# Kernel optimization log

Hardware: AMD Instinct MI355X
Metric: run time of the kernel (lower is better)

## Reference

```python
import jax, jax.numpy as jnp
import numpy as np

N_NODES = 100000
N_EDGES = 3200000
N_FEAT = 128
EMB = 64


def setup_inputs() -> dict:
    key = jax.random.key(0)
    ks = jax.random.split(key, 10)
    x = jax.random.normal(ks[0], (N_NODES, N_FEAT), dtype=jnp.float32)
    edge_index = jax.random.randint(ks[1], (2, N_EDGES), 0, N_NODES, dtype=jnp.int64)
    batch_index = jnp.zeros((N_NODES,), dtype=jnp.int64)
    def glorot(k, fan_in, fan_out):
        s = jnp.sqrt(2.0 / (fan_in + fan_out)).astype(jnp.float32)
        return jax.random.normal(k, (fan_in, fan_out), dtype=jnp.float32) * s
    return {
        "x": x,
        "edge_index": edge_index,
        "batch_index": batch_index,
        "W0": glorot(ks[2], N_FEAT, EMB), "b0": jnp.zeros((EMB,), jnp.float32),
        "W1": glorot(ks[3], EMB, EMB),    "b1": jnp.zeros((EMB,), jnp.float32),
        "W2": glorot(ks[4], EMB, EMB),    "b2": jnp.zeros((EMB,), jnp.float32),
        "W3": glorot(ks[5], EMB, EMB),    "b3": jnp.zeros((EMB,), jnp.float32),
        "Wout": glorot(ks[6], EMB, 1),    "bout": jnp.zeros((1,), jnp.float32),
    }


def _gcn_norm(edge_index, n_nodes):
    # Add self-loops, compute symmetric normalization D^{-1/2} A_hat D^{-1/2}.
    loops = jnp.arange(n_nodes, dtype=edge_index.dtype)
    src = jnp.concatenate([edge_index[0], loops])  # message sources
    dst = jnp.concatenate([edge_index[1], loops])  # aggregation targets
    ones = jnp.ones(src.shape[0], dtype=jnp.float32)
    deg = jax.ops.segment_sum(ones, dst, num_segments=n_nodes)
    dinv = jnp.where(deg > 0, jax.lax.rsqrt(deg), 0.0)
    norm = dinv[src] * dinv[dst]  # [E + N]
    return src, dst, norm


def _gcn_conv(h, src, dst, norm, W, b, n_nodes):
    h = h @ W                              # [N, out]
    msg = h[src] * norm[:, None]           # gather + scale
    agg = jax.ops.segment_sum(msg, dst, num_segments=n_nodes)  # scatter-add
    return agg + b


def reference(x, edge_index, batch_index, W0, b0, W1, b1, W2, b2, W3, b3, Wout, bout):
    n = x.shape[0]
    src, dst, norm = _gcn_norm(edge_index, n)
    y = _gcn_conv(x, src, dst, norm, W0, b0, n)
    y = _gcn_conv(y, src, dst, norm, W1, b1, n)
    y = _gcn_conv(y, src, dst, norm, W2, b2, n)
    y = _gcn_conv(y, src, dst, norm, W3, b3, n)
    out = y @ Wout + bout
    return (out, y)
```

## Files before the change

### kernel.cpp

```cpp
#include <hip/hip_runtime.h>
#include <hip/hip_fp16.h>


#define FEAT 128
#define EMB 64
#define BINSHIFT 8
#define BINSIZE 256
#define NBIN 391
#define CHUNK 8192


__global__ __launch_bounds__(256) void bin_count_k(
    const int* __restrict__ dst, int* __restrict__ bincnt, int E) {
    __shared__ int hist[NBIN];
    int t = threadIdx.x;
    int base = blockIdx.x * CHUNK;
    int end = min(base + CHUNK, E);
    for (int i = t; i < NBIN; i += 256) hist[i] = 0;
    __syncthreads();
    for (int e = base + t; e < end; e += 256)
        atomicAdd(&hist[dst[e] >> BINSHIFT], 1);
    __syncthreads();
    for (int b = t; b < NBIN; b += 256) {
        int c = hist[b];
        if (c > 0) atomicAdd(&bincnt[b], c);
    }
}

__global__ void binscan_k(const int* __restrict__ bincnt, int* __restrict__ binptr,
                          int* __restrict__ bincur, int nbin, int E) {
    __shared__ int s[512];
    int t = threadIdx.x;
    int v = (t < nbin) ? bincnt[t] : 0;
    s[t] = v;
    __syncthreads();
    for (int off = 1; off < 512; off <<= 1) {
        int tv = (t >= off) ? s[t - off] : 0;
        __syncthreads();
        s[t] += tv;
        __syncthreads();
    }
    if (t < nbin) {
        int excl = s[t] - v;
        binptr[t] = excl;
        bincur[t] = excl;
    }
    if (t == 0) binptr[nbin] = E;
}

__global__ __launch_bounds__(256) void bin_edges_k(
    const int* __restrict__ src, const int* __restrict__ dst,
    int* __restrict__ bincur, int* __restrict__ ebuf, int E) {
    __shared__ int hist[NBIN];
    __shared__ int lcur[NBIN];
    int t = threadIdx.x;
    int base = blockIdx.x * CHUNK;
    int end = min(base + CHUNK, E);
    for (int i = t; i < NBIN; i += 256) hist[i] = 0;
    __syncthreads();
    for (int e = base + t; e < end; e += 256)
        atomicAdd(&hist[dst[e] >> BINSHIFT], 1);
    __syncthreads();
    for (int b = t; b < NBIN; b += 256) {
        int c = hist[b];
        lcur[b] = (c > 0) ? atomicAdd(&bincur[b], c) : 0;
    }
    __syncthreads();
    for (int e = base + t; e < end; e += 256) {
        int d = dst[e];
        int bin = d >> BINSHIFT;
        int r = atomicAdd(&lcur[bin], 1);
        ebuf[r] = src[e] | ((d & (BINSIZE - 1)) << 24);
    }
}

__global__ __launch_bounds__(256) void build_csr_k(
    const int* __restrict__ ebuf, const int* __restrict__ binptr,
    int* __restrict__ rowptr, float* __restrict__ dinv,
    int* __restrict__ col, int N, int E, int nbin) {
    __shared__ int lcnt[BINSIZE];
    __shared__ int lscan[BINSIZE];
    __shared__ int lcur[BINSIZE];
    int b = blockIdx.x;
    int t = threadIdx.x;
    int n0 = b << BINSHIFT;
    int e0 = binptr[b];
    int e1 = binptr[b + 1];

    lcnt[t] = 0;
    __syncthreads();
    for (int i = e0 + t; i < e1; i += 256)
        atomicAdd(&lcnt[((unsigned)ebuf[i]) >> 24], 1);
    __syncthreads();

    int v = lcnt[t];
    lscan[t] = v;
    __syncthreads();
    for (int off = 1; off < 256; off <<= 1) {
        int tv = (t >= off) ? lscan[t - off] : 0;
        __syncthreads();
        lscan[t] += tv;
        __syncthreads();
    }
    int excl = e0 + lscan[t] - v;
    lcur[t] = excl;
    if (n0 + t < N) {
        rowptr[n0 + t] = excl;
        dinv[n0 + t] = 1.0f / sqrtf((float)(v + 1));
    }
    if (b == nbin - 1 && t == 0) rowptr[N] = E;
    __syncthreads();

    for (int i = e0 + t; i < e1; i += 256) {
        int w = ebuf[i];
        int dl = ((unsigned)w) >> 24;
        int p = atomicAdd(&lcur[dl], 1);
        col[p] = (w & 0xFFFFFF) << 7;
    }
}

template <int K>
__global__ __launch_bounds__(256, 4) void gemm_scale_k(
    const float* __restrict__ H, const float* __restrict__ W,
    const float* __restrict__ dinv, __half* __restrict__ G, int N) {
    __shared__ float Ws[K * EMB];
    int t = threadIdx.x;
    for (int i = t * 4; i < K * EMB; i += 1024) {
        *(float4*)(Ws + i) = *(const float4*)(W + i);
    }
    __syncthreads();

    int tc = t & 15;
    int tr = t >> 4;
    int j0 = tc * 4;
    int r0 = blockIdx.x * 64 + tr * 4;
    if (r0 >= N) return;

    const float* hp[4];
#pragma unroll
    for (int i = 0; i < 4; i++) {
        int r = (r0 + i < N) ? (r0 + i) : (N - 1);
        hp[i] = H + (size_t)r * K;
    }

    float acc[4][4] = {{0.f}};
    float4 a[4], an[4];
#pragma unroll
    for (int i = 0; i < 4; i++) a[i] = *(const float4*)(hp[i]);

#pragma unroll 1
    for (int k = 0; k < K; k += 4) {
        if (k + 4 < K) {
#pragma unroll
            for (int i = 0; i < 4; i++) an[i] = *(const float4*)(hp[i] + k + 4);
        }
#pragma unroll
        for (int kk = 0; kk < 4; kk++) {
            float4 wv = *(const float4*)(Ws + (k + kk) * EMB + j0);
#pragma unroll
            for (int i = 0; i < 4; i++) {
                float av = (kk == 0) ? a[i].x : (kk == 1) ? a[i].y : (kk == 2) ? a[i].z : a[i].w;
                acc[i][0] = fmaf(av, wv.x, acc[i][0]);
                acc[i][1] = fmaf(av, wv.y, acc[i][1]);
                acc[i][2] = fmaf(av, wv.z, acc[i][2]);
                acc[i][3] = fmaf(av, wv.w, acc[i][3]);
            }
        }
#pragma unroll
        for (int i = 0; i < 4; i++) a[i] = an[i];
    }

#pragma unroll
    for (int i = 0; i < 4; i++) {
        if (r0 + i < N) {
            float s = dinv[r0 + i];
            union { __half2 h2[2]; float2 f2; } o;
            o.h2[0] = __floats2half2_rn(acc[i][0] * s, acc[i][1] * s);
            o.h2[1] = __floats2half2_rn(acc[i][2] * s, acc[i][3] * s);
            *(float2*)(G + (size_t)(r0 + i) * EMB + j0) = o.f2;
        }
    }
}


__device__ __forceinline__ void h8_acc(float (&a)[8], float4 raw) {
    union { float4 f4; __half2 h2[4]; } u;
    u.f4 = raw;
    float2 p0 = __half22float2(u.h2[0]);
    float2 p1 = __half22float2(u.h2[1]);
    float2 p2 = __half22float2(u.h2[2]);
    float2 p3 = __half22float2(u.h2[3]);
    a[0] += p0.x; a[1] += p0.y; a[2] += p1.x; a[3] += p1.y;
    a[4] += p2.x; a[5] += p2.y; a[6] += p3.x; a[7] += p3.y;
}

__device__ __forceinline__ void agg_node8(const __half* __restrict__ G,
                                          const int* __restrict__ coff,
                                          int s, int e, int selfoff,
                                          int grp, int f8, float (&r)[8]) {
    const char* Gb = (const char*)G + f8 * 16;
    float a0[8] = {0.f, 0.f, 0.f, 0.f, 0.f, 0.f, 0.f, 0.f};
    float a1[8] = {0.f, 0.f, 0.f, 0.f, 0.f, 0.f, 0.f, 0.f};
    float a2[8] = {0.f, 0.f, 0.f, 0.f, 0.f, 0.f, 0.f, 0.f};
    float a3[8] = {0.f, 0.f, 0.f, 0.f, 0.f, 0.f, 0.f, 0.f};
    if (grp == 0) h8_acc(a0, *(const float4*)(Gb + selfoff));

    int i = s;
    if (i + 32 <= e) {
        int c0 = coff[i + grp];
        int c1 = coff[i + 8 + grp];
        int c2 = coff[i + 16 + grp];
        int c3 = coff[i + 24 + grp];
        while (true) {
            float4 g0 = *(const float4*)(Gb + (size_t)(unsigned)c0);
            float4 g1 = *(const float4*)(Gb + (size_t)(unsigned)c1);
            float4 g2 = *(const float4*)(Gb + (size_t)(unsigned)c2);
            float4 g3 = *(const float4*)(Gb + (size_t)(unsigned)c3);
            i += 32;
            bool more = (i + 32 <= e);
            if (more) {
                c0 = coff[i + grp];
                c1 = coff[i + 8 + grp];
                c2 = coff[i + 16 + grp];
                c3 = coff[i + 24 + grp];
            }
            h8_acc(a0, g0);
            h8_acc(a1, g1);
            h8_acc(a2, g2);
            h8_acc(a3, g3);
            if (!more) break;
        }
    }
    for (; i + 8 <= e; i += 8) {
        float4 g = *(const float4*)(Gb + (size_t)(unsigned)coff[i + grp]);
        h8_acc(a1, g);
    }
    if (grp < e - i) {
        float4 g = *(const float4*)(Gb + (size_t)(unsigned)coff[i + grp]);
        h8_acc(a2, g);
    }

#pragma unroll
    for (int k = 0; k < 8; k++) {
        float v = (a0[k] + a1[k]) + (a2[k] + a3[k]);
        v += __shfl_xor(v, 8, 64);
        v += __shfl_xor(v, 16, 64);
        v += __shfl_xor(v, 32, 64);
        r[k] = v;
    }
}

__global__ __launch_bounds__(256) void agg_k(
    const __half* __restrict__ G, const float* __restrict__ dinv,
    const int* __restrict__ rowptr, const int* __restrict__ coff,
    const float* __restrict__ bias, float* __restrict__ Hout, int N) {
    int gw = (blockIdx.x * 256 + threadIdx.x) >> 6;
    int lane = threadIdx.x & 63;
    if (gw >= N) return;
    gw = __builtin_amdgcn_readfirstlane(gw);
    int grp = lane >> 3;
    int f8 = lane & 7;
    int s = rowptr[gw], e = rowptr[gw + 1];
    float r[8];
    agg_node8(G, coff, s, e, gw << 7, grp, f8, r);
    if (grp == 0) {
        float d = dinv[gw];
        float4 b0v = *(const float4*)(bias + f8 * 8);
        float4 b1v = *(const float4*)(bias + f8 * 8 + 4);
        float4 lo = make_float4(r[0] * d + b0v.x, r[1] * d + b0v.y,
                                r[2] * d + b0v.z, r[3] * d + b0v.w);
        float4 hi = make_float4(r[4] * d + b1v.x, r[5] * d + b1v.y,
                                r[6] * d + b1v.z, r[7] * d + b1v.w);
        float* o = Hout + (size_t)gw * EMB + f8 * 8;
        *(float4*)o = lo;
        *(float4*)(o + 4) = hi;
    }
}

__global__ __launch_bounds__(256) void agg_final_k(
    const __half* __restrict__ G, const float* __restrict__ dinv,
    const int* __restrict__ rowptr, const int* __restrict__ coff,
    const float* __restrict__ bias, const float* __restrict__ Wout,
    const float* __restrict__ bout, float* __restrict__ Y,
    float* __restrict__ Out, int N) {
    int gw = (blockIdx.x * 256 + threadIdx.x) >> 6;
    int lane = threadIdx.x & 63;
    if (gw >= N) return;
    gw = __builtin_amdgcn_readfirstlane(gw);
    int grp = lane >> 3;
    int f8 = lane & 7;
    int s = rowptr[gw], e = rowptr[gw + 1];
    float r[8];
    agg_node8(G, coff, s, e, gw << 7, grp, f8, r);
    float d = dinv[gw];
    float4 b0v = *(const float4*)(bias + f8 * 8);
    float4 b1v = *(const float4*)(bias + f8 * 8 + 4);
    float v0 = r[0] * d + b0v.x, v1 = r[1] * d + b0v.y;
    float v2 = r[2] * d + b0v.z, v3 = r[3] * d + b0v.w;
    float v4 = r[4] * d + b1v.x, v5 = r[5] * d + b1v.y;
    float v6 = r[6] * d + b1v.z, v7 = r[7] * d + b1v.w;
    if (grp == 0) {
        float* o = Y + (size_t)gw * EMB + f8 * 8;
        *(float4*)o = make_float4(v0, v1, v2, v3);
        *(float4*)(o + 4) = make_float4(v4, v5, v6, v7);
    }
    float4 w0v = *(const float4*)(Wout + f8 * 8);
    float4 w1v = *(const float4*)(Wout + f8 * 8 + 4);
    float p = v0 * w0v.x + v1 * w0v.y + v2 * w0v.z + v3 * w0v.w +
              v4 * w1v.x + v5 * w1v.y + v6 * w1v.z + v7 * w1v.w;
    p += __shfl_xor(p, 1, 8);
    p += __shfl_xor(p, 2, 8);
    p += __shfl_xor(p, 4, 8);
    if (lane == 0) Out[gw] = p + bout[0];
}


extern "C" void kernel_launch(void* const* d_in, const int* in_sizes, int n_in,
                              void* d_out, int out_size, void* d_ws, size_t ws_size,
                              hipStream_t stream) {
    const float* x    = (const float*)d_in[0];
    const int*   ei   = (const int*)d_in[1];
    const float* W0   = (const float*)d_in[3];
    const float* b0   = (const float*)d_in[4];
    const float* W1   = (const float*)d_in[5];
    const float* b1   = (const float*)d_in[6];
    const float* W2   = (const float*)d_in[7];
    const float* b2   = (const float*)d_in[8];
    const float* W3   = (const float*)d_in[9];
    const float* b3   = (const float*)d_in[10];
    const float* Wout = (const float*)d_in[11];
    const float* bout = (const float*)d_in[12];

    const int N = in_sizes[0] / FEAT;
    const int E = in_sizes[1] / 2;
    const int* srcp = ei;
    const int* dstp = ei + E;
    const int nbin = (N + BINSIZE - 1) / BINSIZE;

    const int NP = ((N + 64) + 63) / 64 * 64;
    float* dinv  = (float*)d_ws;
    int* rowptr  = (int*)(dinv + NP);
    int* bincnt  = rowptr + NP;
    int* binptr  = bincnt + 1024;
    int* bincur  = binptr + 1024;
    int* col     = bincur + 1024;
    float* bufA  = (float*)(col + ((E + 63) / 64) * 64);
    int* ebuf    = (int*)bufA;
    __half* Gbuf = (__half*)bufA;

    float* Out = (float*)d_out;
    float* Y   = Out + N;

    const int gemm_blocks = (N + 63) / 64;
    const int agg_blocks  = (N + 3) / 4;
    const int nchunk = (E + CHUNK - 1) / CHUNK;

    hipMemsetAsync(bincnt, 0, 1024 * sizeof(int), stream);
    bin_count_k<<<nchunk, 256, 0, stream>>>(dstp, bincnt, E);
    binscan_k<<<1, 512, 0, stream>>>(bincnt, binptr, bincur, nbin, E);
    bin_edges_k<<<nchunk, 256, 0, stream>>>(srcp, dstp, bincur, ebuf, E);
    build_csr_k<<<nbin, 256, 0, stream>>>(ebuf, binptr, rowptr, dinv, col, N, E, nbin);

    gemm_scale_k<FEAT><<<gemm_blocks, 256, 0, stream>>>(x, W0, dinv, Gbuf, N);
    agg_k<<<agg_blocks, 256, 0, stream>>>(Gbuf, dinv, rowptr, col, b0, Y, N);
    gemm_scale_k<EMB><<<gemm_blocks, 256, 0, stream>>>(Y, W1, dinv, Gbuf, N);
    agg_k<<<agg_blocks, 256, 0, stream>>>(Gbuf, dinv, rowptr, col, b1, Y, N);
    gemm_scale_k<EMB><<<gemm_blocks, 256, 0, stream>>>(Y, W2, dinv, Gbuf, N);
    agg_k<<<agg_blocks, 256, 0, stream>>>(Gbuf, dinv, rowptr, col, b2, Y, N);
    gemm_scale_k<EMB><<<gemm_blocks, 256, 0, stream>>>(Y, W3, dinv, Gbuf, N);
    agg_final_k<<<agg_blocks, 256, 0, stream>>>(Gbuf, dinv, rowptr, col, b3, Wout, bout,
                                                Y, Out, N);
}
```

Measured before the change: 579.3 us.

## Fuse the GEMM and aggregation layers into one persistent cooperative kernel

The four GEMM+scale kernels and four aggregation kernels are replaced by a single persistent cooperative kernel. It loops over row tiles and node groups with grid-stride loops and separates the phases with grid.sync. This removes seven kernel launches and their inter-kernel gaps. In exchange the grid is capped at four 256-thread blocks per CU because of the 32 KB shared weight buffer, which lowers occupancy for the gather-heavy aggregation, and each of the seven grid barriers adds its own cost.

```diff
diff --git a/kernel.cpp b/kernel.cpp
--- a/kernel.cpp
+++ b/kernel.cpp
@@ -1,5 +1,8 @@
 #include <hip/hip_runtime.h>
 #include <hip/hip_fp16.h>
+#include <hip/hip_cooperative_groups.h>
+
+namespace cg = cooperative_groups;
 
 
 #define FEAT 128
@@ -119,65 +122,84 @@
     }
 }
 
+
+struct FusedArgs {
+    const float* x;
+    const float* W0; const float* b0;
+    const float* W1; const float* b1;
+    const float* W2; const float* b2;
+    const float* W3; const float* b3;
+    const float* Wout; const float* bout;
+    const float* dinv;
+    const int* rowptr;
+    const int* coff;
+    __half* G;
+    float* Y;
+    float* Out;
+    int N;
+};
+
 template <int K>
-__global__ __launch_bounds__(256, 4) void gemm_scale_k(
+__device__ __forceinline__ void gemm_phase(
     const float* __restrict__ H, const float* __restrict__ W,
-    const float* __restrict__ dinv, __half* __restrict__ G, int N) {
-    __shared__ float Ws[K * EMB];
+    const float* __restrict__ dinv, __half* __restrict__ G,
+    int N, float* Ws) {
     int t = threadIdx.x;
-    for (int i = t * 4; i < K * EMB; i += 1024) {
+    for (int i = t * 4; i < K * EMB; i += 1024)
         *(float4*)(Ws + i) = *(const float4*)(W + i);
-    }
     __syncthreads();
 
     int tc = t & 15;
     int tr = t >> 4;
     int j0 = tc * 4;
-    int r0 = blockIdx.x * 64 + tr * 4;
-    if (r0 >= N) return;
-
-    const float* hp[4];
-#pragma unroll
-    for (int i = 0; i < 4; i++) {
-        int r = (r0 + i < N) ? (r0 + i) : (N - 1);
-        hp[i] = H + (size_t)r * K;
-    }
-
-    float acc[4][4] = {{0.f}};
-    float4 a[4], an[4];
-#pragma unroll
-    for (int i = 0; i < 4; i++) a[i] = *(const float4*)(hp[i]);
+    int ntile = (N + 63) >> 6;
+
+    for (int tile = blockIdx.x; tile < ntile; tile += gridDim.x) {
+        int r0 = tile * 64 + tr * 4;
+        const float* hp[4];
+#pragma unroll
+        for (int i = 0; i < 4; i++) {
+            int r = (r0 + i < N) ? (r0 + i) : (N - 1);
+            hp[i] = H + (size_t)r * K;
+        }
+
+        float acc[4][4] = {{0.f}};
+        float4 a[4], an[4];
+#pragma unroll
+        for (int i = 0; i < 4; i++) a[i] = *(const float4*)(hp[i]);
 
 #pragma unroll 1
-    for (int k = 0; k < K; k += 4) {
-        if (k + 4 < K) {
-#pragma unroll
-            for (int i = 0; i < 4; i++) an[i] = *(const float4*)(hp[i] + k + 4);
-        }
-#pragma unroll
-        for (int kk = 0; kk < 4; kk++) {
-            float4 wv = *(const float4*)(Ws + (k + kk) * EMB + j0);
-#pragma unroll
-            for (int i = 0; i < 4; i++) {
-                float av = (kk == 0) ? a[i].x : (kk == 1) ? a[i].y : (kk == 2) ? a[i].z : a[i].w;
-                acc[i][0] = fmaf(av, wv.x, acc[i][0]);
-                acc[i][1] = fmaf(av, wv.y, acc[i][1]);
-                acc[i][2] = fmaf(av, wv.z, acc[i][2]);
-                acc[i][3] = fmaf(av, wv.w, acc[i][3]);
+        for (int k = 0; k < K; k += 4) {
+            if (k + 4 < K) {
+#pragma unroll
+                for (int i = 0; i < 4; i++) an[i] = *(const float4*)(hp[i] + k + 4);
             }
-        }
-#pragma unroll
-        for (int i = 0; i < 4; i++) a[i] = an[i];
-    }
-
-#pragma unroll
-    for (int i = 0; i < 4; i++) {
-        if (r0 + i < N) {
-            float s = dinv[r0 + i];
-            union { __half2 h2[2]; float2 f2; } o;
-            o.h2[0] = __floats2half2_rn(acc[i][0] * s, acc[i][1] * s);
-            o.h2[1] = __floats2half2_rn(acc[i][2] * s, acc[i][3] * s);
-            *(float2*)(G + (size_t)(r0 + i) * EMB + j0) = o.f2;
+#pragma unroll
+            for (int kk = 0; kk < 4; kk++) {
+                float4 wv = *(const float4*)(Ws + (k + kk) * EMB + j0);
+#pragma unroll
+                for (int i = 0; i < 4; i++) {
+                    float av = (kk == 0) ? a[i].x : (kk == 1) ? a[i].y
+                             : (kk == 2) ? a[i].z : a[i].w;
+                    acc[i][0] = fmaf(av, wv.x, acc[i][0]);
+                    acc[i][1] = fmaf(av, wv.y, acc[i][1]);
+                    acc[i][2] = fmaf(av, wv.z, acc[i][2]);
+                    acc[i][3] = fmaf(av, wv.w, acc[i][3]);
+                }
+            }
+#pragma unroll
+            for (int i = 0; i < 4; i++) a[i] = an[i];
+        }
+
+#pragma unroll
+        for (int i = 0; i < 4; i++) {
+            if (r0 + i < N) {
+                float s = dinv[r0 + i];
+                union { __half2 h2[2]; float2 f2; } o;
+                o.h2[0] = __floats2half2_rn(acc[i][0] * s, acc[i][1] * s);
+                o.h2[1] = __floats2half2_rn(acc[i][2] * s, acc[i][3] * s);
+                *(float2*)(G + (size_t)(r0 + i) * EMB + j0) = o.f2;
+            }
         }
     }
 }
@@ -250,68 +272,98 @@
     }
 }
 
-__global__ __launch_bounds__(256) void agg_k(
+__device__ __forceinline__ void agg_phase(
     const __half* __restrict__ G, const float* __restrict__ dinv,
     const int* __restrict__ rowptr, const int* __restrict__ coff,
     const float* __restrict__ bias, float* __restrict__ Hout, int N) {
-    int gw = (blockIdx.x * 256 + threadIdx.x) >> 6;
+    int wid = threadIdx.x >> 6;
     int lane = threadIdx.x & 63;
-    if (gw >= N) return;
-    gw = __builtin_amdgcn_readfirstlane(gw);
     int grp = lane >> 3;
     int f8 = lane & 7;
-    int s = rowptr[gw], e = rowptr[gw + 1];
-    float r[8];
-    agg_node8(G, coff, s, e, gw << 7, grp, f8, r);
-    if (grp == 0) {
-        float d = dinv[gw];
-        float4 b0v = *(const float4*)(bias + f8 * 8);
-        float4 b1v = *(const float4*)(bias + f8 * 8 + 4);
-        float4 lo = make_float4(r[0] * d + b0v.x, r[1] * d + b0v.y,
-                                r[2] * d + b0v.z, r[3] * d + b0v.w);
-        float4 hi = make_float4(r[4] * d + b1v.x, r[5] * d + b1v.y,
-                                r[6] * d + b1v.z, r[7] * d + b1v.w);
-        float* o = Hout + (size_t)gw * EMB + f8 * 8;
-        *(float4*)o = lo;
-        *(float4*)(o + 4) = hi;
-    }
-}
-
-__global__ __launch_bounds__(256) void agg_final_k(
+    int ngrp = (N + 3) >> 2;
+    for (int gq = blockIdx.x; gq < ngrp; gq += gridDim.x) {
+        int gw = gq * 4 + wid;
+        if (gw >= N) continue;
+        gw = __builtin_amdgcn_readfirstlane(gw);
+        int s = rowptr[gw], e = rowptr[gw + 1];
+        float r[8];
+        agg_node8(G, coff, s, e, gw << 7, grp, f8, r);
+        if (grp == 0) {
+            float d = dinv[gw];
+            float4 b0v = *(const float4*)(bias + f8 * 8);
+            float4 b1v = *(const float4*)(bias + f8 * 8 + 4);
+            float4 lo = make_float4(r[0] * d + b0v.x, r[1] * d + b0v.y,
+                                    r[2] * d + b0v.z, r[3] * d + b0v.w);
+            float4 hi = make_float4(r[4] * d + b1v.x, r[5] * d + b1v.y,
+                                    r[6] * d + b1v.z, r[7] * d + b1v.w);
+            float* o = Hout + (size_t)gw * EMB + f8 * 8;
+            *(float4*)o = lo;
+            *(float4*)(o + 4) = hi;
+        }
+    }
+}
+
+__device__ __forceinline__ void agg_final_phase(
     const __half* __restrict__ G, const float* __restrict__ dinv,
     const int* __restrict__ rowptr, const int* __restrict__ coff,
     const float* __restrict__ bias, const float* __restrict__ Wout,
     const float* __restrict__ bout, float* __restrict__ Y,
     float* __restrict__ Out, int N) {
-    int gw = (blockIdx.x * 256 + threadIdx.x) >> 6;
+    int wid = threadIdx.x >> 6;
     int lane = threadIdx.x & 63;
-    if (gw >= N) return;
-    gw = __builtin_amdgcn_readfirstlane(gw);
     int grp = lane >> 3;
     int f8 = lane & 7;
-    int s = rowptr[gw], e = rowptr[gw + 1];
-    float r[8];
-    agg_node8(G, coff, s, e, gw << 7, grp, f8, r);
-    float d = dinv[gw];
-    float4 b0v = *(const float4*)(bias + f8 * 8);
-    float4 b1v = *(const float4*)(bias + f8 * 8 + 4);
-    float v0 = r[0] * d + b0v.x, v1 = r[1] * d + b0v.y;
-    float v2 = r[2] * d + b0v.z, v3 = r[3] * d + b0v.w;
-    float v4 = r[4] * d + b1v.x, v5 = r[5] * d + b1v.y;
-    float v6 = r[6] * d + b1v.z, v7 = r[7] * d + b1v.w;
-    if (grp == 0) {
-        float* o = Y + (size_t)gw * EMB + f8 * 8;
-        *(float4*)o = make_float4(v0, v1, v2, v3);
-        *(float4*)(o + 4) = make_float4(v4, v5, v6, v7);
-    }
-    float4 w0v = *(const float4*)(Wout + f8 * 8);
-    float4 w1v = *(const float4*)(Wout + f8 * 8 + 4);
-    float p = v0 * w0v.x + v1 * w0v.y + v2 * w0v.z + v3 * w0v.w +
-              v4 * w1v.x + v5 * w1v.y + v6 * w1v.z + v7 * w1v.w;
-    p += __shfl_xor(p, 1, 8);
-    p += __shfl_xor(p, 2, 8);
-    p += __shfl_xor(p, 4, 8);
-    if (lane == 0) Out[gw] = p + bout[0];
+    int ngrp = (N + 3) >> 2;
+    for (int gq = blockIdx.x; gq < ngrp; gq += gridDim.x) {
+        int gw = gq * 4 + wid;
+        if (gw >= N) continue;
+        gw = __builtin_amdgcn_readfirstlane(gw);
+        int s = rowptr[gw], e = rowptr[gw + 1];
+        float r[8];
+        agg_node8(G, coff, s, e, gw << 7, grp, f8, r);
+        float d = dinv[gw];
+        float4 b0v = *(const float4*)(bias + f8 * 8);
+        float4 b1v = *(const float4*)(bias + f8 * 8 + 4);
+        float v0 = r[0] * d + b0v.x, v1 = r[1] * d + b0v.y;
+        float v2 = r[2] * d + b0v.z, v3 = r[3] * d + b0v.w;
+        float v4 = r[4] * d + b1v.x, v5 = r[5] * d + b1v.y;
+        float v6 = r[6] * d + b1v.z, v7 = r[7] * d + b1v.w;
+        if (grp == 0) {
+            float* o = Y + (size_t)gw * EMB + f8 * 8;
+            *(float4*)o = make_float4(v0, v1, v2, v3);
+            *(float4*)(o + 4) = make_float4(v4, v5, v6, v7);
+        }
+        float4 w0v = *(const float4*)(Wout + f8 * 8);
+        float4 w1v = *(const float4*)(Wout + f8 * 8 + 4);
+        float p = v0 * w0v.x + v1 * w0v.y + v2 * w0v.z + v3 * w0v.w +
+                  v4 * w1v.x + v5 * w1v.y + v6 * w1v.z + v7 * w1v.w;
+        p += __shfl_xor(p, 1, 8);
+        p += __shfl_xor(p, 2, 8);
+        p += __shfl_xor(p, 4, 8);
+        if (lane == 0) Out[gw] = p + bout[0];
+    }
+}
+
+__global__ __launch_bounds__(256, 4) void fused_k(FusedArgs A) {
+    cg::grid_group grid = cg::this_grid();
+    __shared__ float Ws[FEAT * EMB];
+
+    gemm_phase<FEAT>(A.x, A.W0, A.dinv, A.G, A.N, Ws);
+    grid.sync();
+    agg_phase(A.G, A.dinv, A.rowptr, A.coff, A.b0, A.Y, A.N);
+    grid.sync();
+    gemm_phase<EMB>(A.Y, A.W1, A.dinv, A.G, A.N, Ws);
+    grid.sync();
+    agg_phase(A.G, A.dinv, A.rowptr, A.coff, A.b1, A.Y, A.N);
+    grid.sync();
+    gemm_phase<EMB>(A.Y, A.W2, A.dinv, A.G, A.N, Ws);
+    grid.sync();
+    agg_phase(A.G, A.dinv, A.rowptr, A.coff, A.b2, A.Y, A.N);
+    grid.sync();
+    gemm_phase<EMB>(A.Y, A.W3, A.dinv, A.G, A.N, Ws);
+    grid.sync();
+    agg_final_phase(A.G, A.dinv, A.rowptr, A.coff, A.b3, A.Wout, A.bout,
+                    A.Y, A.Out, A.N);
 }
 
 
@@ -351,8 +403,6 @@
     float* Out = (float*)d_out;
     float* Y   = Out + N;
 
-    const int gemm_blocks = (N + 63) / 64;
-    const int agg_blocks  = (N + 3) / 4;
     const int nchunk = (E + CHUNK - 1) / CHUNK;
 
     hipMemsetAsync(bincnt, 0, 1024 * sizeof(int), stream);
@@ -361,13 +411,30 @@
     bin_edges_k<<<nchunk, 256, 0, stream>>>(srcp, dstp, bincur, ebuf, E);
     build_csr_k<<<nbin, 256, 0, stream>>>(ebuf, binptr, rowptr, dinv, col, N, E, nbin);
 
-    gemm_scale_k<FEAT><<<gemm_blocks, 256, 0, stream>>>(x, W0, dinv, Gbuf, N);
-    agg_k<<<agg_blocks, 256, 0, stream>>>(Gbuf, dinv, rowptr, col, b0, Y, N);
-    gemm_scale_k<EMB><<<gemm_blocks, 256, 0, stream>>>(Y, W1, dinv, Gbuf, N);
-    agg_k<<<agg_blocks, 256, 0, stream>>>(Gbuf, dinv, rowptr, col, b1, Y, N);
-    gemm_scale_k<EMB><<<gemm_blocks, 256, 0, stream>>>(Y, W2, dinv, Gbuf, N);
-    agg_k<<<agg_blocks, 256, 0, stream>>>(Gbuf, dinv, rowptr, col, b2, Y, N);
-    gemm_scale_k<EMB><<<gemm_blocks, 256, 0, stream>>>(Y, W3, dinv, Gbuf, N);
-    agg_final_k<<<agg_blocks, 256, 0, stream>>>(Gbuf, dinv, rowptr, col, b3, Wout, bout,
-                                                Y, Out, N);
-}
+    static int nblk = 0;
+    if (nblk == 0) {
+        int bpc = 0;
+        hipError_t err = hipOccupancyMaxActiveBlocksPerMultiprocessor(
+            &bpc, (const void*)fused_k, 256, 0);
+        if (err != hipSuccess || bpc < 1) bpc = 4;
+        if (bpc > 4) bpc = 4;
+        nblk = bpc * 256;
+    }
+    FusedArgs fa;
+    fa.x = x;
+    fa.W0 = W0; fa.b0 = b0;
+    fa.W1 = W1; fa.b1 = b1;
+    fa.W2 = W2; fa.b2 = b2;
+    fa.W3 = W3; fa.b3 = b3;
+    fa.Wout = Wout; fa.bout = bout;
+    fa.dinv = dinv;
+    fa.rowptr = rowptr;
+    fa.coff = col;
+    fa.G = Gbuf;
+    fa.Y = Y;
+    fa.Out = Out;
+    fa.N = N;
+    void* kargs[] = { &fa };
+    hipLaunchCooperativeKernel((void*)fused_k, dim3(nblk), dim3(256),
+                               kargs, 0, stream);
+}
```

New measurement: 1.358 ms. +134.5%, slower.
